# Performance work log

Measured on AMD Instinct MI355X. Metric: run time of the kernel, lower is better.

Reference implementation:

```python
import jax, jax.numpy as jnp
import numpy as np

B, N, NFEAT = 64, 384, 16
E = 3
NHID, NOUT = 128, 128
ST_HID, ST_OUT = 64, 16


def _xavier(key, shape, fan_in, fan_out):
    a = jnp.sqrt(6.0 / (fan_in + fan_out))
    return jax.random.uniform(key, shape, jnp.float32, -a, a)


def setup_inputs() -> dict:
    key = jax.random.key(0)
    ks = jax.random.split(key, 10)
    x = jax.random.normal(ks[0], (B, N, NFEAT), jnp.float32)
    adj = jax.random.uniform(ks[1], (B, E, N, N), jnp.float32)
    emb_w = _xavier(ks[2], (NFEAT, NFEAT), NFEAT, NFEAT)            # Linear(nfeat,nfeat,bias=False)
    gc1_w = _xavier(ks[3], (E, NFEAT, NHID), NFEAT, NHID)           # (edge_dim,in,out)
    gc2_w = _xavier(ks[4], (E, NHID, NHID), NHID, NHID)             # single middle layer (num_layers-2=1)
    gc3_w = _xavier(ks[5], (E, NHID, NOUT), NHID, NOUT)
    st_w1 = _xavier(ks[6], (ST_HID, NOUT), NOUT, ST_HID)            # nn.Linear stores (out,in)
    st_b1 = jnp.zeros((ST_HID,), jnp.float32)
    st_w2 = jnp.full((2 * ST_OUT, ST_HID), 1e-10, jnp.float32)      # init.constant_(linear2.weight, 1e-10)
    st_b2 = jnp.zeros((2 * ST_OUT,), jnp.float32)
    rescale_w = jnp.zeros((1,), jnp.float32)                        # Rescale weight init zero
    return {"x": x, "adj": adj, "emb_w": emb_w, "gc1_w": gc1_w, "gc2_w": gc2_w,
            "gc3_w": gc3_w, "st_w1": st_w1, "st_b1": st_b1, "st_w2": st_w2,
            "st_b2": st_b2, "rescale_w": rescale_w}


def _rgcn_layer(h, adj, W, relu):
    # support: einsum('bid,edh->beih'), aggregate: einsum('beij,bejh->beih'), then sum over e
    support = jnp.einsum('bnd,edh->benh', h, W)
    out = jnp.einsum('bemn,benh->bemh', adj, support)
    if relu:
        out = jax.nn.relu(out)
    return out.sum(axis=1)  # aggregate='sum' over edge types


def reference(x, adj, emb_w, gc1_w, gc2_w, gc3_w, st_w1, st_b1, st_w2, st_b2, rescale_w):
    h = x @ emb_w.T                                   # emb Linear, no bias
    h = _rgcn_layer(h, adj, gc1_w, True)
    h = _rgcn_layer(h, adj, gc2_w, True)
    h = _rgcn_layer(h, adj, gc3_w, False)             # gc3: use_relu=False
    flat = h.reshape(-1, h.shape[-1])                 # (B*N, nout)
    z = jnp.tanh(flat @ st_w1.T + st_b1) @ st_w2.T + st_b2
    s, t = z[:, :ST_OUT], z[:, ST_OUT:]
    s = jnp.exp(rescale_w) * jnp.tanh(s)              # Rescale(tanh(s))
    return jnp.stack([s, t])                          # (2, B*N, ST_OUT)
```

## Files before the change

kernel.cpp:

```cpp
#include <hip/hip_runtime.h>
#include <math.h>

#define ROWS 24576
#define ADJ_BE (384*384)

typedef _Float16 h4v __attribute__((ext_vector_type(4)));
typedef _Float16 h8v __attribute__((ext_vector_type(8)));
typedef float f32x4 __attribute__((ext_vector_type(4)));

#define SPLIT_SCALE 2048.0f
#define INV_SPLIT_SCALE (1.0f / 2048.0f)

__global__ __launch_bounds__(256) void k_embed_adj(const float* __restrict__ x,
        const float* __restrict__ emb_w, const float* __restrict__ adj,
        float* __restrict__ T1) {
    __shared__ float h0L[384][16];
    __shared__ float aT[32][196];
    int t = threadIdx.x;
    int mt = blockIdx.x, e = blockIdx.y, b = blockIdx.z;
    float* embL = &aT[0][0];
    if (t < 64) *(float4*)&embL[4 * t] = *(const float4*)(emb_w + 4 * t);
    __syncthreads();
    const float* xb = x + (size_t)b * 384 * 16;
    for (int rr = t; rr < 384; rr += 256) {
        float xr[16];
        *(float4*)&xr[0]  = *(const float4*)(xb + rr * 16);
        *(float4*)&xr[4]  = *(const float4*)(xb + rr * 16 + 4);
        *(float4*)&xr[8]  = *(const float4*)(xb + rr * 16 + 8);
        *(float4*)&xr[12] = *(const float4*)(xb + rr * 16 + 12);
        float o[16];
#pragma unroll
        for (int d = 0; d < 16; ++d) {
            float acc = 0.f;
#pragma unroll
            for (int k = 0; k < 16; ++k) acc = fmaf(xr[k], embL[d * 16 + k], acc);
            o[d] = acc;
        }
        *(float4*)&h0L[rr][0]  = *(float4*)&o[0];
        *(float4*)&h0L[rr][4]  = *(float4*)&o[4];
        *(float4*)&h0L[rr][8]  = *(float4*)&o[8];
        *(float4*)&h0L[rr][12] = *(float4*)&o[12];
    }
    const float* A = adj + (size_t)(b * 3 + e) * ADJ_BE + (size_t)mt * 192 * 384;
    int tc = t & 3, ty = t >> 2;
    float acc[3][4] = {};
    for (int k0 = 0; k0 < 384; k0 += 32) {
        __syncthreads();
#pragma unroll
        for (int p = 0; p < 6; ++p) {
            int idx = t + p * 256;
            int r = idx >> 3, q = idx & 7;
            float4 v = *(const float4*)(A + (size_t)r * 384 + k0 + q * 4);
            aT[q*4+0][r] = v.x; aT[q*4+1][r] = v.y; aT[q*4+2][r] = v.z; aT[q*4+3][r] = v.w;
        }
        __syncthreads();
#pragma unroll
        for (int k = 0; k < 32; ++k) {
            float2 a01 = *(const float2*)&aT[k][2 * ty];
            float a2 = aT[k][128 + ty];
            float4 bv = *(const float4*)&h0L[k0 + k][4 * tc];
            float bb[4] = {bv.x, bv.y, bv.z, bv.w};
#pragma unroll
            for (int j = 0; j < 4; ++j) {
                acc[0][j] = fmaf(a01.x, bb[j], acc[0][j]);
                acc[1][j] = fmaf(a01.y, bb[j], acc[1][j]);
                acc[2][j] = fmaf(a2,    bb[j], acc[2][j]);
            }
        }
    }
    float* Tp = T1 + (size_t)(b * 3 + e) * (384 * 16) + (size_t)(mt * 192) * 16;
    *(float4*)&Tp[(2 * ty) * 16 + 4 * tc]     = make_float4(acc[0][0], acc[0][1], acc[0][2], acc[0][3]);
    *(float4*)&Tp[(2 * ty + 1) * 16 + 4 * tc] = make_float4(acc[1][0], acc[1][1], acc[1][2], acc[1][3]);
    *(float4*)&Tp[(128 + ty) * 16 + 4 * tc]   = make_float4(acc[2][0], acc[2][1], acc[2][2], acc[2][3]);
}

__global__ __launch_bounds__(256) void k_l1s2(const float* __restrict__ T1,
        const float* __restrict__ W1, float* __restrict__ h1) {
    __shared__ float wL[3][16][128];
    __shared__ float tL[3][64][17];
    int t = threadIdx.x;
    int rt = blockIdx.x;
    int b = rt / 6, m0 = (rt % 6) * 64;
#pragma unroll
    for (int p = 0; p < 6; ++p) {
        int idx = t + p * 256;
        float4 v = *(const float4*)(W1 + (size_t)idx * 4);
        int e = idx / 512, rem = idx % 512;
        int d = rem >> 5, q = rem & 31;
        *(float4*)&wL[e][d][q * 4] = v;
    }
#pragma unroll
    for (int p = 0; p < 3; ++p) {
        int idx = t + p * 256;
        int e = idx >> 8, rem = idx & 255;
        int r = rem >> 2, q = rem & 3;
        float4 v = *(const float4*)(T1 + ((size_t)(b * 3 + e) * 384 + m0 + r) * 16 + q * 4);
        tL[e][r][q*4+0] = v.x; tL[e][r][q*4+1] = v.y; tL[e][r][q*4+2] = v.z; tL[e][r][q*4+3] = v.w;
    }
    __syncthreads();
    int tx = t & 31;
    int ty = t >> 5;
    float tot[8][4] = {};
#pragma unroll
    for (int e = 0; e < 3; ++e) {
        float acc[8][4] = {};
#pragma unroll
        for (int d = 0; d < 16; ++d) {
            float a[8], w[4];
#pragma unroll
            for (int i = 0; i < 8; ++i) a[i] = tL[e][ty + 8 * i][d];
#pragma unroll
            for (int j = 0; j < 4; ++j) w[j] = wL[e][d][tx + 32 * j];
#pragma unroll
            for (int i = 0; i < 8; ++i)
#pragma unroll
                for (int j = 0; j < 4; ++j)
                    acc[i][j] = fmaf(a[i], w[j], acc[i][j]);
        }
#pragma unroll
        for (int i = 0; i < 8; ++i)
#pragma unroll
            for (int j = 0; j < 4; ++j)
                tot[i][j] += fmaxf(acc[i][j], 0.f);
    }
    float* out = h1 + (size_t)rt * 64 * 128;
#pragma unroll
    for (int i = 0; i < 8; ++i)
#pragma unroll
        for (int j = 0; j < 4; ++j)
            out[(ty + 8 * i) * 128 + tx + 32 * j] = tot[i][j];
}

__global__ __launch_bounds__(256) void k_support(const float* __restrict__ hin,
        const float* __restrict__ W, _Float16* __restrict__ Sh, _Float16* __restrict__ Sl) {
    int rt = blockIdx.x, e = blockIdx.y;
    int b = rt / 6, n0 = (rt % 6) * 64;
    const float* Hp = hin + (size_t)rt * 64 * 128;
    const float* Wp = W + (size_t)e * 128 * 128;
    __shared__ float aT[32][68];
    __shared__ float bT[32][132];
    int t = threadIdx.x;
    int tx = t & 15;
    int ty = t >> 4;
    float acc[4][8] = {};
    for (int k0 = 0; k0 < 128; k0 += 32) {
        __syncthreads();
#pragma unroll
        for (int p = 0; p < 2; ++p) {
            int idx = t + p * 256;
            int r = idx >> 3, q = idx & 7;
            float4 v = *(const float4*)(Hp + (size_t)r * 128 + k0 + q * 4);
            aT[q*4+0][r] = v.x; aT[q*4+1][r] = v.y; aT[q*4+2][r] = v.z; aT[q*4+3][r] = v.w;
        }
#pragma unroll
        for (int p = 0; p < 4; ++p) {
            int idx = t + p * 256;
            int r = idx >> 5, q = idx & 31;
            *(float4*)&bT[r][q * 4] = *(const float4*)(Wp + (size_t)(k0 + r) * 128 + q * 4);
        }
        __syncthreads();
#pragma unroll
        for (int k = 0; k < 32; ++k) {
            float4 av = *(const float4*)&aT[k][4 * ty];
            float4 b0 = *(const float4*)&bT[k][4 * tx];
            float4 b1 = *(const float4*)&bT[k][64 + 4 * tx];
            float a[4] = {av.x, av.y, av.z, av.w};
            float bb[8] = {b0.x, b0.y, b0.z, b0.w, b1.x, b1.y, b1.z, b1.w};
#pragma unroll
            for (int i = 0; i < 4; ++i)
#pragma unroll
                for (int j = 0; j < 8; ++j)
                    acc[i][j] = fmaf(a[i], bb[j], acc[i][j]);
        }
    }
    size_t base = (size_t)(b * 3 + e) * 128 * 384;
#pragma unroll
    for (int j = 0; j < 8; ++j) {
        int n = (j < 4) ? (4 * tx + j) : (64 + 4 * tx + j - 4);
        h4v hh, ll;
#pragma unroll
        for (int i = 0; i < 4; ++i) {
            float v = acc[i][j];
            _Float16 h = (_Float16)v;
            hh[i] = h;
            ll[i] = (_Float16)((v - (float)h) * SPLIT_SCALE);
        }
        size_t off = base + (size_t)n * 384 + n0 + 4 * ty;
        *(h4v*)(Sh + off) = hh;
        *(h4v*)(Sl + off) = ll;
    }
}

template <int RELU>
__global__ __launch_bounds__(256, 3) void k_adj_mfma(const float* __restrict__ adj,
        const _Float16* __restrict__ Sh, const _Float16* __restrict__ Sl,
        float* __restrict__ out) {
    int mt = blockIdx.x, e = blockIdx.y, b = blockIdx.z;
    const float* A = adj + (size_t)(b * 3 + e) * ADJ_BE + (size_t)mt * 96 * 384;
    const _Float16* Bh = Sh + (size_t)(b * 3 + e) * 128 * 384;
    const _Float16* Bl = Sl + (size_t)(b * 3 + e) * 128 * 384;
    float* O = out + ((size_t)b * 384 + mt * 96) * 128;

    __shared__ _Float16 Af[2][6][4][16][8];
    __shared__ _Float16 Bf[2][8][4][16][8];

    int t = threadIdx.x;
    int wave = t >> 6, lane = t & 63;
    int l16 = lane & 15, quad = lane >> 4;
    int wm = wave >> 1, wn = wave & 1;

    f32x4 acc0[3][4], acc1[3][4];
#pragma unroll
    for (int i = 0; i < 3; ++i)
#pragma unroll
        for (int j = 0; j < 4; ++j) {
            acc0[i][j] = f32x4{0.f, 0.f, 0.f, 0.f};
            acc1[i][j] = f32x4{0.f, 0.f, 0.f, 0.f};
        }

    for (int k0 = 0; k0 < 384; k0 += 32) {
        __syncthreads();
#pragma unroll
        for (int p = 0; p < 3; ++p) {
            int idx = t + p * 256;
            int r = idx >> 3, q4 = idx & 7;
            float4 v = *(const float4*)(A + (size_t)r * 384 + k0 + 4 * q4);
            h4v hh, ll;
            float vv[4] = {v.x, v.y, v.z, v.w};
#pragma unroll
            for (int c = 0; c < 4; ++c) {
                _Float16 h = (_Float16)vv[c];
                hh[c] = h;
                ll[c] = (_Float16)((vv[c] - (float)h) * SPLIT_SCALE);
            }
            *(h4v*)&Af[0][r >> 4][q4 >> 1][r & 15][(q4 & 1) * 4] = hh;
            *(h4v*)&Af[1][r >> 4][q4 >> 1][r & 15][(q4 & 1) * 4] = ll;
        }
#pragma unroll
        for (int p = 0; p < 2; ++p) {
            int idx = t + p * 256;
            int n = idx >> 2, q8 = idx & 3;
            size_t off = (size_t)n * 384 + k0 + 8 * q8;
            *(h8v*)&Bf[0][n >> 4][q8][n & 15][0] = *(const h8v*)(Bh + off);
            *(h8v*)&Bf[1][n >> 4][q8][n & 15][0] = *(const h8v*)(Bl + off);
        }
        __syncthreads();
        h8v a_h[3], a_l[3];
#pragma unroll
        for (int i = 0; i < 3; ++i) {
            a_h[i] = *(const h8v*)&Af[0][3 * wm + i][quad][l16][0];
            a_l[i] = *(const h8v*)&Af[1][3 * wm + i][quad][l16][0];
        }
#pragma unroll
        for (int j = 0; j < 4; ++j) {
            h8v b_h = *(const h8v*)&Bf[0][4 * wn + j][quad][l16][0];
            h8v b_l = *(const h8v*)&Bf[1][4 * wn + j][quad][l16][0];
#pragma unroll
            for (int i = 0; i < 3; ++i) {
                acc0[i][j] = __builtin_amdgcn_mfma_f32_16x16x32_f16(a_h[i], b_h, acc0[i][j], 0, 0, 0);
                acc1[i][j] = __builtin_amdgcn_mfma_f32_16x16x32_f16(a_h[i], b_l, acc1[i][j], 0, 0, 0);
                acc1[i][j] = __builtin_amdgcn_mfma_f32_16x16x32_f16(a_l[i], b_h, acc1[i][j], 0, 0, 0);
            }
        }
    }
#pragma unroll
    for (int i = 0; i < 3; ++i) {
        int r0 = 48 * wm + 16 * i + quad * 4;
#pragma unroll
        for (int j = 0; j < 4; ++j) {
            int gc = 64 * wn + 16 * j + l16;
#pragma unroll
            for (int reg = 0; reg < 4; ++reg) {
                float v = fmaf(acc1[i][j][reg], INV_SPLIT_SCALE, acc0[i][j][reg]);
                if (RELU) v = fmaxf(v, 0.f);
                atomicAdd(O + (size_t)(r0 + reg) * 128 + gc, v);
            }
        }
    }
}

__global__ void k_zero(float* __restrict__ p, int n4) {
    int i = blockIdx.x * blockDim.x + threadIdx.x;
    if (i < n4) ((float4*)p)[i] = float4{0.f, 0.f, 0.f, 0.f};
}

__global__ __launch_bounds__(256) void k_head(const float* __restrict__ h3,
        const float* __restrict__ st_w1, const float* __restrict__ st_b1,
        const float* __restrict__ st_w2, const float* __restrict__ st_b2,
        const float* __restrict__ rescale_w, float* __restrict__ out) {
    __shared__ float hL[64][132];
    __shared__ float w1L[64][132];
    __shared__ float ytL[64][68];
    __shared__ float w2L[32][68];
    __shared__ float b1L[64], b2L[32];
    int t = threadIdx.x;
    int r0 = blockIdx.x * 64;
#pragma unroll
    for (int p = 0; p < 8; ++p) {
        int idx = t + p * 256;
        int r = idx >> 5, q = idx & 31;
        *(float4*)&hL[r][q * 4] = *(const float4*)(h3 + (size_t)(r0 + r) * 128 + q * 4);
    }
#pragma unroll
    for (int p = 0; p < 8; ++p) {
        int idx = t + p * 256;
        int r = idx >> 5, q = idx & 31;
        *(float4*)&w1L[r][q * 4] = *(const float4*)(st_w1 + (size_t)r * 128 + q * 4);
    }
#pragma unroll
    for (int p = 0; p < 2; ++p) {
        int idx = t + p * 256;
        int r = idx >> 4, q = idx & 15;
        *(float4*)&w2L[r][q * 4] = *(const float4*)(st_w2 + (size_t)r * 64 + q * 4);
    }
    if (t < 64) b1L[t] = st_b1[t];
    else if (t < 96) b2L[t - 64] = st_b2[t - 64];
    __syncthreads();
    int tx = t & 15, ty = t >> 4;
    float acc[4][4] = {};
    for (int d = 0; d < 128; ++d) {
        float a[4], w[4];
#pragma unroll
        for (int i = 0; i < 4; ++i) a[i] = hL[ty + 16 * i][d];
#pragma unroll
        for (int j = 0; j < 4; ++j) w[j] = w1L[tx + 16 * j][d];
#pragma unroll
        for (int i = 0; i < 4; ++i)
#pragma unroll
            for (int j = 0; j < 4; ++j)
                acc[i][j] = fmaf(a[i], w[j], acc[i][j]);
    }
#pragma unroll
    for (int i = 0; i < 4; ++i)
#pragma unroll
        for (int j = 0; j < 4; ++j)
            ytL[ty + 16 * i][tx + 16 * j] = tanhf(acc[i][j] + b1L[tx + 16 * j]);
    __syncthreads();
    int tx8 = t & 7, ty32 = t >> 3;
    float acc2[2][4] = {};
    for (int d = 0; d < 64; ++d) {
        float a[2], w[4];
#pragma unroll
        for (int i = 0; i < 2; ++i) a[i] = ytL[ty32 + 32 * i][d];
#pragma unroll
        for (int j = 0; j < 4; ++j) w[j] = w2L[tx8 + 8 * j][d];
#pragma unroll
        for (int i = 0; i < 2; ++i)
#pragma unroll
            for (int j = 0; j < 4; ++j)
                acc2[i][j] = fmaf(a[i], w[j], acc2[i][j]);
    }
    float er = expf(rescale_w[0]);
#pragma unroll
    for (int i = 0; i < 2; ++i) {
        int r = r0 + ty32 + 32 * i;
#pragma unroll
        for (int j = 0; j < 4; ++j) {
            int c = tx8 + 8 * j;
            float z = acc2[i][j] + b2L[c];
            if (c < 16) out[(size_t)r * 16 + c] = er * tanhf(z);
            else        out[(size_t)(ROWS + r) * 16 + (c - 16)] = z;
        }
    }
}

extern "C" void kernel_launch(void* const* d_in, const int* in_sizes, int n_in,
                              void* d_out, int out_size, void* d_ws, size_t ws_size,
                              hipStream_t stream) {
    const float* x     = (const float*)d_in[0];
    const float* adj   = (const float*)d_in[1];
    const float* emb_w = (const float*)d_in[2];
    const float* gc1   = (const float*)d_in[3];
    const float* gc2   = (const float*)d_in[4];
    const float* gc3   = (const float*)d_in[5];
    const float* st_w1 = (const float*)d_in[6];
    const float* st_b1 = (const float*)d_in[7];
    const float* st_w2 = (const float*)d_in[8];
    const float* st_b2 = (const float*)d_in[9];
    const float* resc  = (const float*)d_in[10];
    float* out = (float*)d_out;
    float* ws  = (float*)d_ws;

    float* T1 = ws;
    float* hA = T1 + 1179648;
    float* hB = hA + 3145728;
    _Float16* Sh = (_Float16*)(hB + 3145728);
    _Float16* Sl = Sh + 9437184;

    k_embed_adj<<<dim3(2, 3, 64), 256, 0, stream>>>(x, emb_w, adj, T1);
    k_l1s2<<<384, 256, 0, stream>>>(T1, gc1, hA);
    k_support<<<dim3(384, 3), 256, 0, stream>>>(hA, gc2, Sh, Sl);
    k_zero<<<3072, 256, 0, stream>>>(hB, 786432);
    k_adj_mfma<1><<<dim3(4, 3, 64), 256, 0, stream>>>(adj, Sh, Sl, hB);
    k_support<<<dim3(384, 3), 256, 0, stream>>>(hB, gc3, Sh, Sl);
    k_zero<<<3072, 256, 0, stream>>>(hA, 786432);
    k_adj_mfma<0><<<dim3(4, 3, 64), 256, 0, stream>>>(adj, Sh, Sl, hA);
    k_head<<<384, 256, 0, stream>>>(hA, st_w1, st_b1, st_w2, st_b2, resc, out);
}
```

Before: 457.5 us.

## Move first adjacency aggregation to split-fp16 MFMA with separate embed kernel

Splits the fused embed+adjacency kernel into two. A small kernel computes the embedding and stores it as transposed hi/lo fp16 pairs. A new kernel aggregates adjacency times embedding with 16x16x32 fp16 MFMA using the hi/lo split, using three MFMAs per step for near-fp32 accuracy. It also uses smaller 64-row tiles for more blocks, replacing the scalar FMA loop that needed a transposed LDS staging. The cost is an extra launch and a temporary buffer reused from hB.

```diff
diff --git a/kernel.cpp b/kernel.cpp
--- a/kernel.cpp
+++ b/kernel.cpp
@@ -11,67 +11,82 @@
 #define SPLIT_SCALE 2048.0f
 #define INV_SPLIT_SCALE (1.0f / 2048.0f)
 
-__global__ __launch_bounds__(256) void k_embed_adj(const float* __restrict__ x,
-        const float* __restrict__ emb_w, const float* __restrict__ adj,
-        float* __restrict__ T1) {
-    __shared__ float h0L[384][16];
-    __shared__ float aT[32][196];
-    int t = threadIdx.x;
-    int mt = blockIdx.x, e = blockIdx.y, b = blockIdx.z;
-    float* embL = &aT[0][0];
+__global__ __launch_bounds__(256) void k_h0split(const float* __restrict__ x,
+        const float* __restrict__ emb_w, _Float16* __restrict__ Hh, _Float16* __restrict__ Hl) {
+    __shared__ float embL[256];
+    int t = threadIdx.x;
     if (t < 64) *(float4*)&embL[4 * t] = *(const float4*)(emb_w + 4 * t);
     __syncthreads();
-    const float* xb = x + (size_t)b * 384 * 16;
-    for (int rr = t; rr < 384; rr += 256) {
-        float xr[16];
-        *(float4*)&xr[0]  = *(const float4*)(xb + rr * 16);
-        *(float4*)&xr[4]  = *(const float4*)(xb + rr * 16 + 4);
-        *(float4*)&xr[8]  = *(const float4*)(xb + rr * 16 + 8);
-        *(float4*)&xr[12] = *(const float4*)(xb + rr * 16 + 12);
-        float o[16];
-#pragma unroll
-        for (int d = 0; d < 16; ++d) {
-            float acc = 0.f;
-#pragma unroll
-            for (int k = 0; k < 16; ++k) acc = fmaf(xr[k], embL[d * 16 + k], acc);
-            o[d] = acc;
-        }
-        *(float4*)&h0L[rr][0]  = *(float4*)&o[0];
-        *(float4*)&h0L[rr][4]  = *(float4*)&o[4];
-        *(float4*)&h0L[rr][8]  = *(float4*)&o[8];
-        *(float4*)&h0L[rr][12] = *(float4*)&o[12];
-    }
-    const float* A = adj + (size_t)(b * 3 + e) * ADJ_BE + (size_t)mt * 192 * 384;
-    int tc = t & 3, ty = t >> 2;
-    float acc[3][4] = {};
+    int gid = blockIdx.x * 256 + t;
+    int b = gid / 384, r = gid % 384;
+    const float* xp = x + (size_t)gid * 16;
+    float xr[16];
+    *(float4*)&xr[0]  = *(const float4*)(xp);
+    *(float4*)&xr[4]  = *(const float4*)(xp + 4);
+    *(float4*)&xr[8]  = *(const float4*)(xp + 8);
+    *(float4*)&xr[12] = *(const float4*)(xp + 12);
+    size_t base = (size_t)b * 16 * 384 + r;
+#pragma unroll
+    for (int d = 0; d < 16; ++d) {
+        float acc = 0.f;
+#pragma unroll
+        for (int k = 0; k < 16; ++k) acc = fmaf(xr[k], embL[d * 16 + k], acc);
+        _Float16 h = (_Float16)acc;
+        Hh[base + (size_t)d * 384] = h;
+        Hl[base + (size_t)d * 384] = (_Float16)((acc - (float)h) * SPLIT_SCALE);
+    }
+}
+
+__global__ __launch_bounds__(256) void k_adj16(const float* __restrict__ adj,
+        const _Float16* __restrict__ Hh, const _Float16* __restrict__ Hl,
+        float* __restrict__ T1) {
+    int mt = blockIdx.x, e = blockIdx.y, b = blockIdx.z;
+    const float* A = adj + (size_t)(b * 3 + e) * ADJ_BE + (size_t)mt * 64 * 384;
+    const _Float16* BH = Hh + (size_t)b * 16 * 384;
+    const _Float16* BL = Hl + (size_t)b * 16 * 384;
+
+    __shared__ _Float16 Af[2][4][4][16][8];
+
+    int t = threadIdx.x;
+    int wave = t >> 6, lane = t & 63;
+    int l16 = lane & 15, quad = lane >> 4;
+
+    f32x4 acc0 = f32x4{0.f, 0.f, 0.f, 0.f};
+    f32x4 acc1 = f32x4{0.f, 0.f, 0.f, 0.f};
+
     for (int k0 = 0; k0 < 384; k0 += 32) {
         __syncthreads();
 #pragma unroll
-        for (int p = 0; p < 6; ++p) {
+        for (int p = 0; p < 2; ++p) {
             int idx = t + p * 256;
-            int r = idx >> 3, q = idx & 7;
-            float4 v = *(const float4*)(A + (size_t)r * 384 + k0 + q * 4);
-            aT[q*4+0][r] = v.x; aT[q*4+1][r] = v.y; aT[q*4+2][r] = v.z; aT[q*4+3][r] = v.w;
-        }
-        __syncthreads();
-#pragma unroll
-        for (int k = 0; k < 32; ++k) {
-            float2 a01 = *(const float2*)&aT[k][2 * ty];
-            float a2 = aT[k][128 + ty];
-            float4 bv = *(const float4*)&h0L[k0 + k][4 * tc];
-            float bb[4] = {bv.x, bv.y, bv.z, bv.w};
-#pragma unroll
-            for (int j = 0; j < 4; ++j) {
-                acc[0][j] = fmaf(a01.x, bb[j], acc[0][j]);
-                acc[1][j] = fmaf(a01.y, bb[j], acc[1][j]);
-                acc[2][j] = fmaf(a2,    bb[j], acc[2][j]);
+            int r = idx >> 3, q4 = idx & 7;
+            float4 v = *(const float4*)(A + (size_t)r * 384 + k0 + 4 * q4);
+            h4v hh, ll;
+            float vv[4] = {v.x, v.y, v.z, v.w};
+#pragma unroll
+            for (int c = 0; c < 4; ++c) {
+                _Float16 h = (_Float16)vv[c];
+                hh[c] = h;
+                ll[c] = (_Float16)((vv[c] - (float)h) * SPLIT_SCALE);
             }
-        }
-    }
-    float* Tp = T1 + (size_t)(b * 3 + e) * (384 * 16) + (size_t)(mt * 192) * 16;
-    *(float4*)&Tp[(2 * ty) * 16 + 4 * tc]     = make_float4(acc[0][0], acc[0][1], acc[0][2], acc[0][3]);
-    *(float4*)&Tp[(2 * ty + 1) * 16 + 4 * tc] = make_float4(acc[1][0], acc[1][1], acc[1][2], acc[1][3]);
-    *(float4*)&Tp[(128 + ty) * 16 + 4 * tc]   = make_float4(acc[2][0], acc[2][1], acc[2][2], acc[2][3]);
+            *(h4v*)&Af[0][r >> 4][q4 >> 1][r & 15][(q4 & 1) * 4] = hh;
+            *(h4v*)&Af[1][r >> 4][q4 >> 1][r & 15][(q4 & 1) * 4] = ll;
+        }
+        h8v b_h = *(const h8v*)(BH + (size_t)l16 * 384 + k0 + 8 * quad);
+        h8v b_l = *(const h8v*)(BL + (size_t)l16 * 384 + k0 + 8 * quad);
+        __syncthreads();
+        h8v a_h = *(const h8v*)&Af[0][wave][quad][l16][0];
+        h8v a_l = *(const h8v*)&Af[1][wave][quad][l16][0];
+        acc0 = __builtin_amdgcn_mfma_f32_16x16x32_f16(a_h, b_h, acc0, 0, 0, 0);
+        acc1 = __builtin_amdgcn_mfma_f32_16x16x32_f16(a_h, b_l, acc1, 0, 0, 0);
+        acc1 = __builtin_amdgcn_mfma_f32_16x16x32_f16(a_l, b_h, acc1, 0, 0, 0);
+    }
+    float* Tp = T1 + ((size_t)(b * 3 + e) * 384 + (size_t)mt * 64 + wave * 16) * 16;
+#pragma unroll
+    for (int reg = 0; reg < 4; ++reg) {
+        float v = fmaf(acc1[reg], INV_SPLIT_SCALE, acc0[reg]);
+        Tp[(quad * 4 + reg) * 16 + l16] = v;
+    }
 }
 
 __global__ __launch_bounds__(256) void k_l1s2(const float* __restrict__ T1,
@@ -386,8 +401,11 @@
     float* hB = hA + 3145728;
     _Float16* Sh = (_Float16*)(hB + 3145728);
     _Float16* Sl = Sh + 9437184;
-
-    k_embed_adj<<<dim3(2, 3, 64), 256, 0, stream>>>(x, emb_w, adj, T1);
+    _Float16* Hh = (_Float16*)hB;
+    _Float16* Hl = Hh + 393216;
+
+    k_h0split<<<96, 256, 0, stream>>>(x, emb_w, Hh, Hl);
+    k_adj16<<<dim3(6, 3, 64), 256, 0, stream>>>(adj, Hh, Hl, T1);
     k_l1s2<<<384, 256, 0, stream>>>(T1, gc1, hA);
     k_support<<<dim3(384, 3), 256, 0, stream>>>(hA, gc2, Sh, Sl);
     k_zero<<<3072, 256, 0, stream>>>(hB, 786432);
```

New measurement: 441.3 us. 1.04x faster.
